# Optimization experiments

Measured on AMD Instinct MI355X. Metric: run time of the kernel, lower is better.

The kernel has to match this reference:

```python
import jax, jax.numpy as jnp
import numpy as np

NLAG = 300  # int(maxlag/dt) = int(3.0/0.01)


def setup_inputs() -> dict:
    key = jax.random.key(0)
    k1, k2 = jax.random.split(key)
    data1 = jax.random.normal(k1, (64, 32, 3000), dtype=jnp.float32)
    data2 = jax.random.normal(k2, (64, 32, 3000), dtype=jnp.float32)
    return {"data1": data1, "data2": data2}


def reference(data1, data2):
    # Time-domain full cross-correlation via grouped conv1d (PyTorch conv1d
    # does correlation, no kernel flip; lax.conv_general_dilated matches).
    nb, nc, nt = data1.shape
    g = nb * nc
    lhs = data1.reshape(1, g, nt)          # (N=1, C=g, T)
    rhs = data2.reshape(g, 1, nt)          # (O=g, I=1, T) one filter per group
    xcor = jax.lax.conv_general_dilated(
        lhs, rhs,
        window_strides=(1,),
        padding=[(NLAG + 1, NLAG + 1)],
        feature_group_count=g,
        dimension_numbers=("NCH", "OIH", "NCH"),
    )  # (1, g, 2*NLAG+3)
    return xcor.reshape(nb, nc, -1)
```

## Files before the change

### kernel.cpp

```cpp
#include <hip/hip_runtime.h>


#define NT    3000
#define NOUT  603
#define CHPB  4
#define BLOCK 256

#define L1B  6784
#define L2B  8192
#define CHB  (L1B + L2B)
#define TOTB (CHB * CHPB)

typedef short bf16x8 __attribute__((ext_vector_type(8)));
typedef float f32x4  __attribute__((ext_vector_type(4)));

static __device__ __forceinline__ uint f2bf(float f) {
    union { float f; uint u; } a; a.f = f;
    return (a.u + 0x7fffu + ((a.u >> 16) & 1u)) >> 16;
}

__global__ __launch_bounds__(BLOCK, 2) void xcorr_mfma(
    const float* __restrict__ d1g, const float* __restrict__ d2g,
    float* __restrict__ out)
{
    __shared__ __align__(16) unsigned char smem[TOTB];
    const int tid = threadIdx.x;
    const int chBase = blockIdx.x * CHPB;

    for (int i = tid; i < CHPB * 196; i += BLOCK) {
        const int c = i / 196, j = i % 196;
        const int dw = (j < 152) ? j : (1652 + (j - 152));
        ((uint*)(smem + c * CHB))[dw] = 0u;
    }
    for (int i = tid; i < CHPB * 548; i += BLOCK) {
        const int c = i / 548, j = i % 548;
        const int dw = (j < 384) ? j : (1884 + (j - 384));
        ((uint*)(smem + c * CHB + L1B))[dw] = 0u;
    }

    for (int i = tid; i < CHPB * 750; i += BLOCK) {
        const int c = i / 750, j = i % 750;
        const float4 v = *(const float4*)(d1g + (size_t)(chBase + c) * NT + 4 * j);
        uint2 p;
        p.x = f2bf(v.x) | (f2bf(v.y) << 16);
        p.y = f2bf(v.z) | (f2bf(v.w) << 16);
        *(uint2*)(smem + c * CHB + 608 + 8 * j) = p;
    }
    for (int i = tid; i < CHPB * 750; i += BLOCK) {
        const int c = i / 750, j = i % 750;
        const float4 v = *(const float4*)(d2g + (size_t)(chBase + c) * NT + 4 * j);
        uint2 p;
        p.x = f2bf(v.x) | (f2bf(v.y) << 16);
        p.y = f2bf(v.z) | (f2bf(v.w) << 16);
        *(uint2*)(smem + c * CHB + L1B + 1536 + 8 * j) = p;
    }
    __syncthreads();

    const int wid = tid >> 6, lane = tid & 63;
    const int q = lane >> 4, r = lane & 15;
    const uint* lA = (const uint*)(smem + wid * CHB);
    const uint* lB = (const uint*)(smem + wid * CHB + L1B);

    f32x4 a00 = {0.f,0.f,0.f,0.f};
    f32x4 a10 = {0.f,0.f,0.f,0.f};
    f32x4 a01 = {0.f,0.f,0.f,0.f};
    f32x4 a11 = {0.f,0.f,0.f,0.f};

    int4 fifo[16];
    {
        const int dbP = 256 + 4 * q - 16 * r;
        #pragma unroll
        for (int s = 0; s < 16; ++s)
            fifo[s] = *(const int4*)(lB + dbP + 16 * s);
    }

    int da = 130 + 4 * q + r;
    int db = 512 + 4 * q - 16 * r;

    for (int jo = 0; jo < 6; ++jo) {
        #pragma unroll
        for (int u = 0; u < 16; ++u) {
            const uint* pa = lA + da;
            const uint Dm1 = pa[-1], D0 = pa[0], D1 = pa[1], D2 = pa[2], D3 = pa[3];

            union { uint w[4]; bf16x8 v; int4 i4; } f1, f0, g0, g1;
            f1.w[0] = D0; f1.w[1] = D1; f1.w[2] = D2; f1.w[3] = D3;
            f0.w[0] = (Dm1 >> 16) | (D0 << 16);
            f0.w[1] = (D0  >> 16) | (D1 << 16);
            f0.w[2] = (D1  >> 16) | (D2 << 16);
            f0.w[3] = (D2  >> 16) | (D3 << 16);

            g0.i4 = *(const int4*)(lB + db);
            g1.i4 = fifo[u];
            fifo[u] = g0.i4;

            a00 = __builtin_amdgcn_mfma_f32_16x16x32_bf16(f0.v, g0.v, a00, 0, 0, 0);
            a10 = __builtin_amdgcn_mfma_f32_16x16x32_bf16(f1.v, g0.v, a10, 0, 0, 0);
            a01 = __builtin_amdgcn_mfma_f32_16x16x32_bf16(f0.v, g1.v, a01, 0, 0, 0);
            a11 = __builtin_amdgcn_mfma_f32_16x16x32_bf16(f1.v, g1.v, a11, 0, 0, 0);

            da += 16; db += 16;
        }
    }

    float* o = out + (size_t)(chBase + wid) * NOUT;
    {
        const int X = 32 * r + 8 * q;
        float4 s0 = {a00[0], a10[0], a00[1], a10[1]};
        float4 s1 = {a00[2], a10[2], a00[3], a10[3]};
        *(float4*)(o + X)     = s0;
        *(float4*)(o + X + 4) = s1;
    }
    {
        const int X = 512 + 32 * r + 8 * q;
        if (X + 7 < NOUT) {
            float4 s0 = {a01[0], a11[0], a01[1], a11[1]};
            float4 s1 = {a01[2], a11[2], a01[3], a11[3]};
            *(float4*)(o + X)     = s0;
            *(float4*)(o + X + 4) = s1;
        } else if (X < NOUT) {
            const float v[8] = {a01[0], a11[0], a01[1], a11[1],
                                a01[2], a11[2], a01[3], a11[3]};
            #pragma unroll
            for (int e = 0; e < 8; ++e)
                if (X + e < NOUT) o[X + e] = v[e];
        }
    }
}

extern "C" void kernel_launch(void* const* d_in, const int* in_sizes, int n_in,
                              void* d_out, int out_size, void* d_ws, size_t ws_size,
                              hipStream_t stream) {
    const float* d1 = (const float*)d_in[0];
    const float* d2 = (const float*)d_in[1];
    float* out = (float*)d_out;
    const int nChannels = in_sizes[0] / NT;
    const int grid = nChannels / CHPB;
    xcorr_mfma<<<grid, BLOCK, 0, stream>>>(d1, d2, out);
}
```

Baseline: 25.69 us.

## Use one wave per channel and stream input staging alongside MFMA loop

Changes the launch from 4-wave blocks handling four channels to single-wave blocks handling one channel each, which removes the block-wide barrier. Instead of staging the whole signal into LDS before computing, only the first chunks are staged up front. Each outer iteration prefetches the next 256-dword chunk from global memory, converts it to bf16 after the MFMA batch, and writes it to LDS, so global loads overlap compute. The aim is to hide load latency and raise occupancy with smaller LDS per block. The cost is more blocks and no sharing of staging work across waves. The correctness of the in-loop prefetch relies on lookahead distances staying ahead of the reads.

```diff
diff --git a/kernel.cpp b/kernel.cpp
--- a/kernel.cpp
+++ b/kernel.cpp
@@ -3,13 +3,9 @@
 
 #define NT    3000
 #define NOUT  603
-#define CHPB  4
-#define BLOCK 256
-
-#define L1B  6784
-#define L2B  8192
-#define CHB  (L1B + L2B)
-#define TOTB (CHB * CHPB)
+#define BLOCK 64
+#define L1DW  1696
+#define L2DW  2048
 
 typedef short bf16x8 __attribute__((ext_vector_type(8)));
 typedef float f32x4  __attribute__((ext_vector_type(4)));
@@ -23,87 +19,125 @@
     const float* __restrict__ d1g, const float* __restrict__ d2g,
     float* __restrict__ out)
 {
-    __shared__ __align__(16) unsigned char smem[TOTB];
-    const int tid = threadIdx.x;
-    const int chBase = blockIdx.x * CHPB;
+    __shared__ __align__(16) uint l1[L1DW];
+    __shared__ __align__(16) uint l2[L2DW];
 
-    for (int i = tid; i < CHPB * 196; i += BLOCK) {
-        const int c = i / 196, j = i % 196;
-        const int dw = (j < 152) ? j : (1652 + (j - 152));
-        ((uint*)(smem + c * CHB))[dw] = 0u;
+    const int lane = threadIdx.x & 63;
+    const int q = lane >> 4, r = lane & 15;
+    const int ch = blockIdx.x;
+    const float* __restrict__ g1 = d1g + (size_t)ch * NT;
+    const float* __restrict__ g2 = d2g + (size_t)ch * NT;
+
+    for (int j = lane; j < 196; j += BLOCK) {
+        const int dw = (j < 152) ? j : 1652 + (j - 152);
+        l1[dw] = 0u;
     }
-    for (int i = tid; i < CHPB * 548; i += BLOCK) {
-        const int c = i / 548, j = i % 548;
-        const int dw = (j < 384) ? j : (1884 + (j - 384));
-        ((uint*)(smem + c * CHB + L1B))[dw] = 0u;
+    for (int j = lane; j < 548; j += BLOCK) {
+        const int dw = (j < 384) ? j : 1884 + (j - 384);
+        l2[dw] = 0u;
     }
 
-    for (int i = tid; i < CHPB * 750; i += BLOCK) {
-        const int c = i / 750, j = i % 750;
-        const float4 v = *(const float4*)(d1g + (size_t)(chBase + c) * NT + 4 * j);
-        uint2 p;
-        p.x = f2bf(v.x) | (f2bf(v.y) << 16);
-        p.y = f2bf(v.z) | (f2bf(v.w) << 16);
-        *(uint2*)(smem + c * CHB + 608 + 8 * j) = p;
+    auto stageA = [&](int dstart) {
+        const int d = dstart + 4 * lane;
+        const int e0 = 2 * (d - 152);
+        if (e0 < NT) {
+            const float4 v = *(const float4*)(g1 + e0);
+            const float4 w = *(const float4*)(g1 + e0 + 4);
+            int4 p;
+            p.x = (int)(f2bf(v.x) | (f2bf(v.y) << 16));
+            p.y = (int)(f2bf(v.z) | (f2bf(v.w) << 16));
+            p.z = (int)(f2bf(w.x) | (f2bf(w.y) << 16));
+            p.w = (int)(f2bf(w.z) | (f2bf(w.w) << 16));
+            *(int4*)(l1 + d) = p;
+        }
+    };
+    auto stageB = [&](int dstart) {
+        const int d = dstart + 4 * lane;
+        const int e0 = 2 * (d - 384);
+        if (e0 < NT) {
+            const float4 v = *(const float4*)(g2 + e0);
+            const float4 w = *(const float4*)(g2 + e0 + 4);
+            int4 p;
+            p.x = (int)(f2bf(v.x) | (f2bf(v.y) << 16));
+            p.y = (int)(f2bf(v.z) | (f2bf(v.w) << 16));
+            p.z = (int)(f2bf(w.x) | (f2bf(w.y) << 16));
+            p.w = (int)(f2bf(w.z) | (f2bf(w.w) << 16));
+            *(int4*)(l2 + d) = p;
+        }
+    };
+
+    stageA(152); stageA(408);
+    stageB(384); stageB(640);
+
+    int4 fifo[16];
+    {
+        const int dbP = 256 + 4 * q - 16 * r;
+        #pragma unroll
+        for (int s = 0; s < 16; ++s)
+            fifo[s] = *(const int4*)(l2 + dbP + 16 * s);
     }
-    for (int i = tid; i < CHPB * 750; i += BLOCK) {
-        const int c = i / 750, j = i % 750;
-        const float4 v = *(const float4*)(d2g + (size_t)(chBase + c) * NT + 4 * j);
-        uint2 p;
-        p.x = f2bf(v.x) | (f2bf(v.y) << 16);
-        p.y = f2bf(v.z) | (f2bf(v.w) << 16);
-        *(uint2*)(smem + c * CHB + L1B + 1536 + 8 * j) = p;
-    }
-    __syncthreads();
-
-    const int wid = tid >> 6, lane = tid & 63;
-    const int q = lane >> 4, r = lane & 15;
-    const uint* lA = (const uint*)(smem + wid * CHB);
-    const uint* lB = (const uint*)(smem + wid * CHB + L1B);
 
     f32x4 a00 = {0.f,0.f,0.f,0.f};
     f32x4 a10 = {0.f,0.f,0.f,0.f};
     f32x4 a01 = {0.f,0.f,0.f,0.f};
     f32x4 a11 = {0.f,0.f,0.f,0.f};
 
-    int4 fifo[16];
-    {
-        const int dbP = 256 + 4 * q - 16 * r;
-        #pragma unroll
-        for (int s = 0; s < 16; ++s)
-            fifo[s] = *(const int4*)(lB + dbP + 16 * s);
-    }
-
     int da = 130 + 4 * q + r;
     int db = 512 + 4 * q - 16 * r;
+    int aPre = 664, bPre = 896;
 
-    for (int jo = 0; jo < 6; ++jo) {
+    for (int c = 0; c < 6; ++c) {
+        const int dA = aPre + 4 * lane, eA = 2 * (dA - 152);
+        const int dB = bPre + 4 * lane, eB = 2 * (dB - 384);
+        const bool okA = eA < NT, okB = eB < NT;
+        float4 va0, va1, vb0, vb1;
+        if (okA) { va0 = *(const float4*)(g1 + eA); va1 = *(const float4*)(g1 + eA + 4); }
+        if (okB) { vb0 = *(const float4*)(g2 + eB); vb1 = *(const float4*)(g2 + eB + 4); }
+
         #pragma unroll
         for (int u = 0; u < 16; ++u) {
-            const uint* pa = lA + da;
+            const uint* pa = (const uint*)l1 + da;
             const uint Dm1 = pa[-1], D0 = pa[0], D1 = pa[1], D2 = pa[2], D3 = pa[3];
 
-            union { uint w[4]; bf16x8 v; int4 i4; } f1, f0, g0, g1;
+            union { uint w[4]; bf16x8 v; int4 i4; } f1, f0, g0, g1u;
             f1.w[0] = D0; f1.w[1] = D1; f1.w[2] = D2; f1.w[3] = D3;
             f0.w[0] = (Dm1 >> 16) | (D0 << 16);
             f0.w[1] = (D0  >> 16) | (D1 << 16);
             f0.w[2] = (D1  >> 16) | (D2 << 16);
             f0.w[3] = (D2  >> 16) | (D3 << 16);
 
-            g0.i4 = *(const int4*)(lB + db);
-            g1.i4 = fifo[u];
+            g0.i4 = *(const int4*)((const uint*)l2 + db);
+            g1u.i4 = fifo[u];
             fifo[u] = g0.i4;
 
-            a00 = __builtin_amdgcn_mfma_f32_16x16x32_bf16(f0.v, g0.v, a00, 0, 0, 0);
-            a10 = __builtin_amdgcn_mfma_f32_16x16x32_bf16(f1.v, g0.v, a10, 0, 0, 0);
-            a01 = __builtin_amdgcn_mfma_f32_16x16x32_bf16(f0.v, g1.v, a01, 0, 0, 0);
-            a11 = __builtin_amdgcn_mfma_f32_16x16x32_bf16(f1.v, g1.v, a11, 0, 0, 0);
+            a00 = __builtin_amdgcn_mfma_f32_16x16x32_bf16(f0.v, g0.v,  a00, 0, 0, 0);
+            a10 = __builtin_amdgcn_mfma_f32_16x16x32_bf16(f1.v, g0.v,  a10, 0, 0, 0);
+            a01 = __builtin_amdgcn_mfma_f32_16x16x32_bf16(f0.v, g1u.v, a01, 0, 0, 0);
+            a11 = __builtin_amdgcn_mfma_f32_16x16x32_bf16(f1.v, g1u.v, a11, 0, 0, 0);
 
             da += 16; db += 16;
         }
+
+        if (okA) {
+            int4 p;
+            p.x = (int)(f2bf(va0.x) | (f2bf(va0.y) << 16));
+            p.y = (int)(f2bf(va0.z) | (f2bf(va0.w) << 16));
+            p.z = (int)(f2bf(va1.x) | (f2bf(va1.y) << 16));
+            p.w = (int)(f2bf(va1.z) | (f2bf(va1.w) << 16));
+            *(int4*)(l1 + dA) = p;
+        }
+        if (okB) {
+            int4 p;
+            p.x = (int)(f2bf(vb0.x) | (f2bf(vb0.y) << 16));
+            p.y = (int)(f2bf(vb0.z) | (f2bf(vb0.w) << 16));
+            p.z = (int)(f2bf(vb1.x) | (f2bf(vb1.y) << 16));
+            p.w = (int)(f2bf(vb1.z) | (f2bf(vb1.w) << 16));
+            *(int4*)(l2 + dB) = p;
+        }
+        aPre += 256; bPre += 256;
     }
 
-    float* o = out + (size_t)(chBase + wid) * NOUT;
+    float* o = out + (size_t)ch * NOUT;
     {
         const int X = 32 * r + 8 * q;
         float4 s0 = {a00[0], a10[0], a00[1], a10[1]};
@@ -135,6 +169,5 @@
     const float* d2 = (const float*)d_in[1];
     float* out = (float*)d_out;
     const int nChannels = in_sizes[0] / NT;
-    const int grid = nChannels / CHPB;
-    xcorr_mfma<<<grid, BLOCK, 0, stream>>>(d1, d2, out);
+    xcorr_mfma<<<nChannels, BLOCK, 0, stream>>>(d1, d2, out);
 }
```

Result: faster. 21.78 us (-15.2%).

## Split each channel's correlation across two waves with LDS reduction

Applied to the files above, without the earlier changes.

Each block now handles two channels instead of four, and two waves share each channel, each covering half of the 96-step reduction. The partial accumulators are combined through shared memory before the store. The register FIFO for the second B fragment is replaced by a direct second LDS read, and launch bounds rise to allow four blocks per CU. The aim is more blocks and shorter per-wave dependency chains for better latency hiding. The cost is extra LDS traffic, two barriers and a reduction step.

```diff
diff --git a/kernel.cpp b/kernel.cpp
--- a/kernel.cpp
+++ b/kernel.cpp
@@ -3,7 +3,7 @@
 
 #define NT    3000
 #define NOUT  603
-#define CHPB  4
+#define CHPB  2
 #define BLOCK 256
 
 #define L1B  6784
@@ -19,7 +19,7 @@
     return (a.u + 0x7fffu + ((a.u >> 16) & 1u)) >> 16;
 }
 
-__global__ __launch_bounds__(BLOCK, 2) void xcorr_mfma(
+__global__ __launch_bounds__(BLOCK, 4) void xcorr_mfma(
     const float* __restrict__ d1g, const float* __restrict__ d2g,
     float* __restrict__ out)
 {
@@ -57,53 +57,63 @@
     __syncthreads();
 
     const int wid = tid >> 6, lane = tid & 63;
+    const int c = wid >> 1, h = wid & 1;
     const int q = lane >> 4, r = lane & 15;
-    const uint* lA = (const uint*)(smem + wid * CHB);
-    const uint* lB = (const uint*)(smem + wid * CHB + L1B);
+    const uint* lA = (const uint*)(smem + c * CHB);
+    const uint* lB = (const uint*)(smem + c * CHB + L1B);
 
     f32x4 a00 = {0.f,0.f,0.f,0.f};
     f32x4 a10 = {0.f,0.f,0.f,0.f};
     f32x4 a01 = {0.f,0.f,0.f,0.f};
     f32x4 a11 = {0.f,0.f,0.f,0.f};
 
-    int4 fifo[16];
-    {
-        const int dbP = 256 + 4 * q - 16 * r;
-        #pragma unroll
-        for (int s = 0; s < 16; ++s)
-            fifo[s] = *(const int4*)(lB + dbP + 16 * s);
+    int da = 130 + 4 * q + r + 768 * h;
+    int db = 512 + 4 * q - 16 * r + 768 * h;
+
+    #pragma unroll 4
+    for (int i = 0; i < 48; ++i) {
+        const uint* pa = lA + da;
+        const uint Dm1 = pa[-1], D0 = pa[0], D1 = pa[1], D2 = pa[2], D3 = pa[3];
+
+        union { uint w[4]; bf16x8 v; int4 i4; } f1, f0, g0, g1u;
+        f1.w[0] = D0; f1.w[1] = D1; f1.w[2] = D2; f1.w[3] = D3;
+        f0.w[0] = (Dm1 >> 16) | (D0 << 16);
+        f0.w[1] = (D0  >> 16) | (D1 << 16);
+        f0.w[2] = (D1  >> 16) | (D2 << 16);
+        f0.w[3] = (D2  >> 16) | (D3 << 16);
+
+        g0.i4  = *(const int4*)(lB + db);
+        g1u.i4 = *(const int4*)(lB + db - 256);
+
+        a00 = __builtin_amdgcn_mfma_f32_16x16x32_bf16(f0.v, g0.v,  a00, 0, 0, 0);
+        a10 = __builtin_amdgcn_mfma_f32_16x16x32_bf16(f1.v, g0.v,  a10, 0, 0, 0);
+        a01 = __builtin_amdgcn_mfma_f32_16x16x32_bf16(f0.v, g1u.v, a01, 0, 0, 0);
+        a11 = __builtin_amdgcn_mfma_f32_16x16x32_bf16(f1.v, g1u.v, a11, 0, 0, 0);
+
+        da += 16; db += 16;
     }
 
-    int da = 130 + 4 * q + r;
-    int db = 512 + 4 * q - 16 * r;
+    __syncthreads();
+    uint* S = (uint*)(smem + c * CHB);
+    const int soff = lane * 17;
+    if (h == 1) {
+        *(f32x4*)(S + soff)      = a00;
+        *(f32x4*)(S + soff + 4)  = a10;
+        *(f32x4*)(S + soff + 8)  = a01;
+        *(f32x4*)(S + soff + 12) = a11;
+    }
+    __syncthreads();
+    if (h == 1) return;
 
-    for (int jo = 0; jo < 6; ++jo) {
-        #pragma unroll
-        for (int u = 0; u < 16; ++u) {
-            const uint* pa = lA + da;
-            const uint Dm1 = pa[-1], D0 = pa[0], D1 = pa[1], D2 = pa[2], D3 = pa[3];
-
-            union { uint w[4]; bf16x8 v; int4 i4; } f1, f0, g0, g1;
-            f1.w[0] = D0; f1.w[1] = D1; f1.w[2] = D2; f1.w[3] = D3;
-            f0.w[0] = (Dm1 >> 16) | (D0 << 16);
-            f0.w[1] = (D0  >> 16) | (D1 << 16);
-            f0.w[2] = (D1  >> 16) | (D2 << 16);
-            f0.w[3] = (D2  >> 16) | (D3 << 16);
-
-            g0.i4 = *(const int4*)(lB + db);
-            g1.i4 = fifo[u];
-            fifo[u] = g0.i4;
-
-            a00 = __builtin_amdgcn_mfma_f32_16x16x32_bf16(f0.v, g0.v, a00, 0, 0, 0);
-            a10 = __builtin_amdgcn_mfma_f32_16x16x32_bf16(f1.v, g0.v, a10, 0, 0, 0);
-            a01 = __builtin_amdgcn_mfma_f32_16x16x32_bf16(f0.v, g1.v, a01, 0, 0, 0);
-            a11 = __builtin_amdgcn_mfma_f32_16x16x32_bf16(f1.v, g1.v, a11, 0, 0, 0);
-
-            da += 16; db += 16;
-        }
+    {
+        const f32x4 b00 = *(const f32x4*)(S + soff);
+        const f32x4 b10 = *(const f32x4*)(S + soff + 4);
+        const f32x4 b01 = *(const f32x4*)(S + soff + 8);
+        const f32x4 b11 = *(const f32x4*)(S + soff + 12);
+        a00 += b00; a10 += b10; a01 += b01; a11 += b11;
     }
 
-    float* o = out + (size_t)(chBase + wid) * NOUT;
+    float* o = out + (size_t)(chBase + c) * NOUT;
     {
         const int X = 32 * r + 8 * q;
         float4 s0 = {a00[0], a10[0], a00[1], a10[1]};
```

After: 24.76 us. 1.04x faster.
